# Kernel tuning notes

Hardware: AMD Instinct MI355X
Metric: run time of the kernel (lower is better)

## Reference

```python
import jax, jax.numpy as jnp
import numpy as np

B, C, L, H, W = 4, 128, 8, 64, 64

def setup_inputs() -> dict:
    key = jax.random.key(0)
    ks = jax.random.split(key, 9)
    s = 0.05
    return {
        'feats': jax.random.normal(ks[0], (B, C, L, H, W), jnp.float32),
        'proj_w': jax.random.normal(ks[1], (C, C, L), jnp.float32) * s,  # Conv3d kernel (band,1,1) collapsing l
        'proj_b': jax.random.normal(ks[2], (C,), jnp.float32) * s,
        'w1': jax.random.normal(ks[3], (C, C), jnp.float32) * s,
        'b1': jax.random.normal(ks[4], (C,), jnp.float32) * s,
        'w2': jax.random.normal(ks[5], (C, C), jnp.float32) * s,
        'b2': jax.random.normal(ks[6], (C,), jnp.float32) * s,
        'w3': jax.random.normal(ks[7], (C, C), jnp.float32) * s,
        'b3': jax.random.normal(ks[8], (C,), jnp.float32) * s,
        'alpha': jnp.zeros((1,), jnp.float32),
    }

def reference(feats, proj_w, proj_b, w1, b1, w2, b2, w3, b3, alpha):
    b, c, l, h, w = feats.shape
    hw = h * w
    # CVT3D_2D_SA: 3D->2D projection, conv3d kernel (l,1,1) then squeeze
    f2d = jnp.einsum('bclhw,ocl->bohw', feats, proj_w) + proj_b[None, :, None, None]
    # 1x1 conv projections -> (b, c, hw)
    x = f2d.reshape(b, c, hw)
    q = jnp.einsum('bcn,oc->bon', x, w1) + b1[None, :, None]
    k = jnp.einsum('bcn,oc->bon', x, w2) + b2[None, :, None]
    v = jnp.einsum('bcn,oc->bon', x, w3) + b3[None, :, None]
    # scores[b,n,m] = sum_c q[b,c,n] * k[b,c,m]; softmax over m (dim=-1)
    scores = jnp.einsum('bcn,bcm->bnm', q, k)
    attn = jax.nn.softmax(scores, axis=-1)
    # feat_e[b,c,n] = sum_m v[b,c,m] * attn[b,n,m]
    feat_e = jnp.einsum('bcm,bnm->bcn', v, attn).reshape(b, c, h, w)
    # original computes out = alpha*feat_e + f2d but returns feat_e
    return feat_e
```

## Files before the change

kernel.cpp:

```cpp
#include <hip/hip_runtime.h>
#include <stdint.h>

typedef _Float16 h8 __attribute__((ext_vector_type(8)));
typedef _Float16 h4 __attribute__((ext_vector_type(4)));
typedef float f32x4 __attribute__((ext_vector_type(4)));
typedef uint32_t u32x4 __attribute__((ext_vector_type(4)));

#if __has_builtin(__builtin_amdgcn_exp2f)
#define EXP2(x) __builtin_amdgcn_exp2f(x)
#else
#define EXP2(x) exp2f(x)
#endif

#define WS_PWH  0u
#define WS_WH   262144u
#define WS_BC   600064u
#define WS_F2D  1048576u
#define WS_OP   5242880u
#define WS_QKVT 38797312u
#define WS_VT   47185920u
#define WS_MLM  0u
#define WS_MLL  524288u

__device__ __forceinline__ void gll16(const void* g, void* l) {
  __builtin_amdgcn_global_load_lds((const __attribute__((address_space(1))) unsigned int*)g,
                                   (__attribute__((address_space(3))) unsigned int*)l, 16, 0, 0);
}

__global__ void k_cvt(const float* __restrict__ pw, const float* __restrict__ pb,
                      const float* __restrict__ w1, const float* __restrict__ b1,
                      const float* __restrict__ w2, const float* __restrict__ b2,
                      const float* __restrict__ w3, const float* __restrict__ b3,
                      _Float16* __restrict__ PWh, _Float16* __restrict__ Wh,
                      float* __restrict__ bc)
{
  const float LOG2E = 1.4426950408889634f;
  int idx = blockIdx.x * 256 + threadIdx.x;
  if (idx < 131072) {
    PWh[idx] = (_Float16)pw[idx];
  } else {
    int j = idx - 131072;
    if (j < 49152) {
      int g = j >> 14, rem = j & 16383;
      const float* wg = (g == 0) ? w1 : (g == 1 ? w2 : w3);
      float v = wg[rem];
      if (g == 0) v *= LOG2E;
      Wh[j] = (_Float16)v;
    }
  }
  if (idx < 384) {
    int g = idx >> 7, o = idx & 127;
    const float* wg = (g == 0) ? w1 : (g == 1 ? w2 : w3);
    const float* bg = (g == 0) ? b1 : (g == 1 ? b2 : b3);
    float s = bg[o];
    for (int c = 0; c < 128; ++c) s += wg[o * 128 + c] * pb[c];
    if (g == 0) s *= LOG2E;
    bc[idx] = s;
  }
}

#define FG1_LDS 51200
__global__ __launch_bounds__(256) void k_fg1(const float* __restrict__ feats,
                                             const _Float16* __restrict__ PWh,
                                             _Float16* __restrict__ f2d)
{
  extern __shared__ char smem[];
  const int t = threadIdx.x, lane = t & 63, w = t >> 6;
  const int lo = lane & 15, hi = lane >> 4;
  const int n0 = blockIdx.x * 32, b = blockIdx.y;
  const int wr = w >> 1, wc = w & 1;
  const char* pwc = (const char*)PWh;

  float4 areg[2];
  auto loadA = [&](int s) {
    #pragma unroll
    for (int p = 0; p < 2; ++p) {
      int i = t + p * 256, row = i >> 3, slot = i & 7;
      areg[p] = *(const float4*)(feats + ((size_t)(b * 1024 + s * 64 + row)) * 4096 + n0 + slot * 4);
    }
  };
  auto writeA = [&](int buf) {
    char* base = smem + buf * 9216;
    #pragma unroll
    for (int p = 0; p < 2; ++p) {
      int i = t + p * 256, row = i >> 3, slot = i & 7;
      *(float4*)(base + row * 144 + slot * 16) = areg[p];
    }
  };
  auto gllB = [&](int s, int buf) {
    char* base = smem + 18432 + buf * 16384;
    #pragma unroll
    for (int q = 0; q < 4; ++q) {
      int o = (w * 4 + q) * 8 + (lane >> 3);
      int slot = lane & 7;
      gll16(pwc + (size_t)o * 2048 + s * 128 + ((slot * 16) ^ ((o & 7) << 4)),
            base + (w * 4 + q) * 1024);
    }
  };

  const f32x4 zero4 = {0.f, 0.f, 0.f, 0.f};
  f32x4 acc[4];
  #pragma unroll
  for (int j2 = 0; j2 < 4; ++j2) acc[j2] = zero4;

  loadA(0); writeA(0); gllB(0, 0);
  for (int s = 0; s < 16; ++s) {
    __syncthreads();
    if (s < 15) { loadA(s + 1); gllB(s + 1, (s + 1) & 1); }
    const char* fb = smem + (s & 1) * 9216;
    const char* pb_ = smem + 18432 + (s & 1) * 16384;
    #pragma unroll
    for (int kk = 0; kk < 2; ++kk) {
      const int nl = wr * 16 + lo;
      float f0 = *(const float*)(fb + (kk * 32 + hi * 8 + 0) * 144 + nl * 4);
      float f1 = *(const float*)(fb + (kk * 32 + hi * 8 + 1) * 144 + nl * 4);
      float f2 = *(const float*)(fb + (kk * 32 + hi * 8 + 2) * 144 + nl * 4);
      float f3 = *(const float*)(fb + (kk * 32 + hi * 8 + 3) * 144 + nl * 4);
      float f4 = *(const float*)(fb + (kk * 32 + hi * 8 + 4) * 144 + nl * 4);
      float f5 = *(const float*)(fb + (kk * 32 + hi * 8 + 5) * 144 + nl * 4);
      float f6 = *(const float*)(fb + (kk * 32 + hi * 8 + 6) * 144 + nl * 4);
      float f7 = *(const float*)(fb + (kk * 32 + hi * 8 + 7) * 144 + nl * 4);
      u32x4 ua = { __builtin_bit_cast(uint32_t, __builtin_amdgcn_cvt_pkrtz(f0, f1)),
                   __builtin_bit_cast(uint32_t, __builtin_amdgcn_cvt_pkrtz(f2, f3)),
                   __builtin_bit_cast(uint32_t, __builtin_amdgcn_cvt_pkrtz(f4, f5)),
                   __builtin_bit_cast(uint32_t, __builtin_amdgcn_cvt_pkrtz(f6, f7)) };
      h8 af = __builtin_bit_cast(h8, ua);
      h8 bf[4];
      #pragma unroll
      for (int j2 = 0; j2 < 4; ++j2) {
        int o = wc * 64 + j2 * 16 + lo;
        bf[j2] = *(const h8*)(pb_ + o * 128 + ((kk * 64 + hi * 16) ^ ((o & 7) << 4)));
      }
      #pragma unroll
      for (int j2 = 0; j2 < 4; ++j2)
        acc[j2] = __builtin_amdgcn_mfma_f32_16x16x32_f16(af, bf[j2], acc[j2], 0, 0, 0);
    }
    if (s < 15) writeA((s + 1) & 1);
  }

  #pragma unroll
  for (int j2 = 0; j2 < 4; ++j2) {
    int o = wc * 64 + j2 * 16 + lo;
    #pragma unroll
    for (int r = 0; r < 4; ++r) {
      int n = n0 + wr * 16 + hi * 4 + r;
      f2d[((size_t)(b * 4096 + n)) * 128 + o] = (_Float16)acc[j2][r];
    }
  }
}

__global__ void k_gemm2(const _Float16* __restrict__ f2d, const _Float16* __restrict__ Wh,
                        const float* __restrict__ bc, _Float16* __restrict__ qkvt,
                        _Float16* __restrict__ vt)
{
  extern __shared__ char smem[];
  const int t = threadIdx.x, lane = t & 63, w = t >> 6;
  const int lo = lane & 15, hi = lane >> 4;
  const int bx = blockIdx.x, n0 = blockIdx.y * 128, b = blockIdx.z;
  const int wr = w >> 1, wc = w & 1;
  const int nb = wr * 64, ob = wc * 64;
  const char* f2c = (const char*)f2d;

  #pragma unroll
  for (int q = 0; q < 8; ++q) {
    int c = w * 8 + q;
    int row = c * 4 + (lane >> 4);
    int col = ((lane & 15) * 16) ^ ((row & 7) << 4);
    gll16(f2c + ((size_t)(b * 4096 + n0 + row)) * 256 + col, smem + c * 1024);
    gll16((const char*)Wh + (size_t)(bx * 128 + row) * 256 + col, smem + 32768 + c * 1024);
  }
  __syncthreads();

  const f32x4 zero4 = {0.f, 0.f, 0.f, 0.f};
  f32x4 acc[4][4];
  #pragma unroll
  for (int i2 = 0; i2 < 4; ++i2)
    #pragma unroll
    for (int j2 = 0; j2 < 4; ++j2) acc[i2][j2] = zero4;

  #pragma unroll
  for (int kk = 0; kk < 4; ++kk) {
    const int cb = kk * 64 + hi * 16;
    h8 af[4], bf[4];
    #pragma unroll
    for (int i2 = 0; i2 < 4; ++i2) {
      int row = nb + i2 * 16 + lo;
      af[i2] = *(const h8*)(smem + row * 256 + (cb ^ ((row & 7) << 4)));
    }
    #pragma unroll
    for (int j2 = 0; j2 < 4; ++j2) {
      int row = ob + j2 * 16 + lo;
      bf[j2] = *(const h8*)(smem + 32768 + row * 256 + (cb ^ ((row & 7) << 4)));
    }
    #pragma unroll
    for (int i2 = 0; i2 < 4; ++i2)
      #pragma unroll
      for (int j2 = 0; j2 < 4; ++j2)
        acc[i2][j2] = __builtin_amdgcn_mfma_f32_16x16x32_f16(af[i2], bf[j2], acc[i2][j2], 0, 0, 0);
  }

  if (bx < 2) {
    #pragma unroll
    for (int j2 = 0; j2 < 4; ++j2) {
      int o = bx * 128 + ob + j2 * 16 + lo;
      float bias = bc[o];
      #pragma unroll
      for (int i2 = 0; i2 < 4; ++i2)
        #pragma unroll
        for (int r = 0; r < 4; ++r) {
          int n = n0 + nb + i2 * 16 + hi * 4 + r;
          qkvt[((size_t)(b * 4096 + n)) * 256 + o] = (_Float16)(acc[i2][j2][r] + bias);
        }
    }
  } else {
    __syncthreads();
    #pragma unroll
    for (int j2 = 0; j2 < 4; ++j2) {
      int o = ob + j2 * 16 + lo;
      float bias = bc[256 + o];
      #pragma unroll
      for (int i2 = 0; i2 < 4; ++i2) {
        int nl = nb + i2 * 16 + hi * 4;
        h4 v4;
        #pragma unroll
        for (int r = 0; r < 4; ++r) v4[r] = (_Float16)(acc[i2][j2][r] + bias);
        *(h4*)(smem + o * 272 + nl * 2) = v4;
      }
    }
    __syncthreads();
    #pragma unroll
    for (int p2 = 0; p2 < 8; ++p2) {
      int i = t + p2 * 256, d = i >> 4, ch = i & 15;
      uint4 v = *(const uint4*)(smem + d * 272 + ch * 16);
      *(uint4*)((char*)vt + ((size_t)(b * 128 + d)) * 8192 + (n0 + ch * 8) * 2) = v;
    }
  }
}

#define ATT_LDS 65536
__global__ __launch_bounds__(512, 4) void k_attn_part(const _Float16* __restrict__ qkvt,
                                                      const _Float16* __restrict__ vt,
                                                      _Float16* __restrict__ opart,
                                                      float* __restrict__ mlm,
                                                      float* __restrict__ mll)
{
  extern __shared__ char smem[];
  const int t = threadIdx.x, lane = t & 63, w = t >> 6;
  const int lo = lane & 15, hi = lane >> 4;
  const int id = blockIdx.x;
  const int vid = (id & 7) * 128 + (id >> 3);
  const int qt = vid & 31, bp = vid >> 5;
  const int b = bp >> 3, p = bp & 7;
  const int n0 = qt * 128;
  const char* qbase = (const char*)qkvt + (size_t)b * 4096 * 512;
  const char* vbase = (const char*)vt + (size_t)b * 128 * 8192;

  h8 bq[4];
  {
    const char* qr = qbase + (size_t)(n0 + w * 16 + lo) * 512;
    #pragma unroll
    for (int dk = 0; dk < 4; ++dk) bq[dk] = *(const h8*)(qr + dk * 64 + hi * 16);
  }

  int koff[2], voff[2], dst_[2];
  #pragma unroll
  for (int q = 0; q < 2; ++q) {
    int c = w * 2 + q;
    int krow = c * 4 + (lane >> 4);
    koff[q] = krow * 512 + 256 + (((lane & 15) * 16) ^ ((krow & 7) << 4));
    int d = c * 8 + (lane >> 3);
    voff[q] = d * 8192 + (((lane & 7) * 16) ^ ((d & 7) << 4));
    dst_[q] = c * 1024;
  }

  auto stage = [&](int m0, int buf) {
    char* kb = smem + buf * 32768;
    char* vb = kb + 16384;
    #pragma unroll
    for (int q = 0; q < 2; ++q) {
      gll16(qbase + (size_t)m0 * 512 + koff[q], kb + dst_[q]);
      gll16(vbase + (size_t)m0 * 2 + voff[q], vb + dst_[q]);
    }
  };

  const f32x4 zero4 = {0.f, 0.f, 0.f, 0.f};
  float m_run = -1e30f, l_run = 0.f;
  f32x4 oacc[8];
  #pragma unroll
  for (int dt = 0; dt < 8; ++dt) oacc[dt] = zero4;

  const int slA = (hi & 1) * 32 + lo, slB = slA + 16;
  const bool up = (hi & 2) != 0;

  stage(p * 512, 0);
  __syncthreads();

  for (int it = 0; it < 8; ++it) {
    const int buf = it & 1;
    if (it < 7) stage(p * 512 + (it + 1) * 64, buf ^ 1);

    const char* kb = smem + buf * 32768;
    const char* vb = kb + 16384;

    f32x4 s[4];
    #pragma unroll
    for (int mt = 0; mt < 4; ++mt) s[mt] = zero4;
    __builtin_amdgcn_s_setprio(1);
    #pragma unroll
    for (int mt = 0; mt < 4; ++mt) {
      #pragma unroll
      for (int dk = 0; dk < 4; ++dk) {
        int row = mt * 16 + lo;
        h8 ak = *(const h8*)(kb + row * 256 + ((dk * 64 + hi * 16) ^ ((row & 7) << 4)));
        s[mt] = __builtin_amdgcn_mfma_f32_16x16x32_f16(ak, bq[dk], s[mt], 0, 0, 0);
      }
    }
    __builtin_amdgcn_s_setprio(0);

    float mxl = fmaxf(fmaxf(fmaxf(s[0][0], s[0][1]), fmaxf(s[0][2], s[0][3])),
                      fmaxf(fmaxf(s[1][0], s[1][1]), fmaxf(s[1][2], s[1][3])));
    mxl = fmaxf(mxl, fmaxf(fmaxf(fmaxf(s[2][0], s[2][1]), fmaxf(s[2][2], s[2][3])),
                           fmaxf(fmaxf(s[3][0], s[3][1]), fmaxf(s[3][2], s[3][3]))));
    if (__any(mxl > m_run + 8.f)) {
      float mq = fmaxf(mxl, __shfl_xor(mxl, 16));
      mq = fmaxf(mq, __shfl_xor(mq, 32));
      float mnew = fmaxf(m_run, mq);
      float scn = EXP2(m_run - mnew);
      m_run = mnew;
      l_run *= scn;
      #pragma unroll
      for (int dt = 0; dt < 8; ++dt) oacc[dt] *= scn;
    }

    uint32_t pk[4][2];
    float rs = 0.f;
    #pragma unroll
    for (int mt = 0; mt < 4; ++mt) {
      float p0 = EXP2(s[mt][0] - m_run), p1 = EXP2(s[mt][1] - m_run);
      float p2 = EXP2(s[mt][2] - m_run), p3 = EXP2(s[mt][3] - m_run);
      rs += (p0 + p1) + (p2 + p3);
      pk[mt][0] = __builtin_bit_cast(uint32_t, __builtin_amdgcn_cvt_pkrtz(p0, p1));
      pk[mt][1] = __builtin_bit_cast(uint32_t, __builtin_amdgcn_cvt_pkrtz(p2, p3));
    }
    l_run += rs;

    #pragma unroll
    for (int kk2 = 0; kk2 < 2; ++kk2) {
      uint32_t w0a = __shfl(pk[kk2 * 2][0], slA), w0b = __shfl(pk[kk2 * 2 + 1][0], slA);
      uint32_t w1a = __shfl(pk[kk2 * 2][1], slA), w1b = __shfl(pk[kk2 * 2 + 1][1], slA);
      uint32_t w2a = __shfl(pk[kk2 * 2][0], slB), w2b = __shfl(pk[kk2 * 2 + 1][0], slB);
      uint32_t w3a = __shfl(pk[kk2 * 2][1], slB), w3b = __shfl(pk[kk2 * 2 + 1][1], slB);
      u32x4 bw = { up ? w0b : w0a, up ? w1b : w1a, up ? w2b : w2a, up ? w3b : w3a };
      h8 bpf = __builtin_bit_cast(h8, bw);
      __builtin_amdgcn_s_setprio(1);
      #pragma unroll
      for (int dt = 0; dt < 8; ++dt) {
        int d = dt * 16 + lo;
        h8 av = *(const h8*)(vb + d * 128 + (((kk2 * 4 + hi) * 16) ^ ((d & 7) << 4)));
        oacc[dt] = __builtin_amdgcn_mfma_f32_16x16x32_f16(av, bpf, oacc[dt], 0, 0, 0);
      }
      __builtin_amdgcn_s_setprio(0);
    }

    if (it < 7) __syncthreads();
  }

  l_run += __shfl_xor(l_run, 16);
  l_run += __shfl_xor(l_run, 32);
  float invl = 1.0f / l_run;
  _Float16* oph = opart + ((size_t)(p * 4 + b) * 128) * 4096;
  const int ncol = n0 + w * 16 + lo;
  #pragma unroll
  for (int dt = 0; dt < 8; ++dt)
    #pragma unroll
    for (int r = 0; r < 4; ++r) {
      int d = dt * 16 + hi * 4 + r;
      oph[(size_t)d * 4096 + ncol] = (_Float16)(oacc[dt][r] * invl);
    }
  if (hi == 0) {
    size_t mlbase = (size_t)(p * 4 + b) * 4096 + ncol;
    mlm[mlbase] = m_run;
    mll[mlbase] = l_run;
  }
}

__global__ void k_reduce(const _Float16* __restrict__ opart, const float* __restrict__ mlm,
                         const float* __restrict__ mll, float* __restrict__ out)
{
  int idx = blockIdx.x * 256 + threadIdx.x;
  int n4 = idx & 1023, d = (idx >> 10) & 127, b = idx >> 17;
  int n0 = n4 * 4;
  f32x4 m[8], lv[8];
  #pragma unroll
  for (int p = 0; p < 8; ++p) {
    size_t mb = (size_t)(p * 4 + b) * 4096 + n0;
    m[p]  = *(const f32x4*)(mlm + mb);
    lv[p] = *(const f32x4*)(mll + mb);
  }
  f32x4 M = m[0];
  #pragma unroll
  for (int p = 1; p < 8; ++p)
    #pragma unroll
    for (int j = 0; j < 4; ++j) M[j] = fmaxf(M[j], m[p][j]);
  f32x4 denom = {0.f, 0.f, 0.f, 0.f}, num = {0.f, 0.f, 0.f, 0.f};
  #pragma unroll
  for (int p = 0; p < 8; ++p) {
    h4 o = *(const h4*)(opart + ((size_t)((p * 4 + b) * 128 + d)) * 4096 + n0);
    #pragma unroll
    for (int j = 0; j < 4; ++j) {
      float wgt = lv[p][j] * EXP2(m[p][j] - M[j]);
      denom[j] += wgt;
      num[j]   += (float)o[j] * wgt;
    }
  }
  f32x4 r;
  #pragma unroll
  for (int j = 0; j < 4; ++j) r[j] = num[j] / denom[j];
  *(f32x4*)(out + ((size_t)(b * 128 + d)) * 4096 + n0) = r;
}

extern "C" void kernel_launch(void* const* d_in, const int* in_sizes, int n_in,
                              void* d_out, int out_size, void* d_ws, size_t ws_size,
                              hipStream_t stream)
{
  const float* feats = (const float*)d_in[0];
  const float* pw = (const float*)d_in[1];
  const float* pb = (const float*)d_in[2];
  const float* w1 = (const float*)d_in[3];
  const float* b1 = (const float*)d_in[4];
  const float* w2 = (const float*)d_in[5];
  const float* b2 = (const float*)d_in[6];
  const float* w3 = (const float*)d_in[7];
  const float* b3 = (const float*)d_in[8];
  char* ws = (char*)d_ws;
  _Float16* PWh = (_Float16*)(ws + WS_PWH);
  _Float16* Wh = (_Float16*)(ws + WS_WH);
  float* bc = (float*)(ws + WS_BC);
  _Float16* f2d = (_Float16*)(ws + WS_F2D);
  _Float16* qkvt = (_Float16*)(ws + WS_QKVT);
  _Float16* vt = (_Float16*)(ws + WS_VT);
  _Float16* opart = (_Float16*)(ws + WS_OP);
  float* mlm = (float*)(ws + WS_MLM);
  float* mll = (float*)(ws + WS_MLL);
  float* out = (float*)d_out;

  hipLaunchKernelGGL(k_cvt, dim3(704), dim3(256), 0, stream,
                     pw, pb, w1, b1, w2, b2, w3, b3, PWh, Wh, bc);
  hipLaunchKernelGGL(k_fg1, dim3(128, 4), dim3(256), FG1_LDS, stream, feats, PWh, f2d);
  hipLaunchKernelGGL(k_gemm2, dim3(3, 32, 4), dim3(256), 65536, stream, f2d, Wh, bc, qkvt, vt);
  hipLaunchKernelGGL(k_attn_part, dim3(1024), dim3(512), ATT_LDS, stream, qkvt, vt, opart, mlm, mll);
  hipLaunchKernelGGL(k_reduce, dim3(2048), dim3(256), 0, stream, opart, mlm, mll, out);
}
```

Baseline: 108.1 us.

## Software-pipeline attention loop with 32-key tiles and triple-buffered K

Restructures the attention partial kernel to process 32-key tiles instead of 64, triple-buffering K and double-buffering V in a smaller LDS footprint. The QK^T MFMAs for the next tile are issued before the softmax and PV of the current tile, so matrix work overlaps the exponentials and shuffles. The LDS swizzle and staging layout are rewritten so each thread issues one 16-byte load per operand. This doubles the number of iterations and barriers, adds register pressure from the extra score accumulators, and the smaller LDS use may allow more blocks per CU.

```diff
diff --git a/kernel.cpp b/kernel.cpp
--- a/kernel.cpp
+++ b/kernel.cpp
@@ -237,7 +237,7 @@
   }
 }
 
-#define ATT_LDS 65536
+#define ATT_LDS 40960
 __global__ __launch_bounds__(512, 4) void k_attn_part(const _Float16* __restrict__ qkvt,
                                                       const _Float16* __restrict__ vt,
                                                       _Float16* __restrict__ opart,
@@ -262,25 +262,18 @@
     for (int dk = 0; dk < 4; ++dk) bq[dk] = *(const h8*)(qr + dk * 64 + hi * 16);
   }
 
-  int koff[2], voff[2], dst_[2];
-  #pragma unroll
-  for (int q = 0; q < 2; ++q) {
-    int c = w * 2 + q;
-    int krow = c * 4 + (lane >> 4);
-    koff[q] = krow * 512 + 256 + (((lane & 15) * 16) ^ ((krow & 7) << 4));
-    int d = c * 8 + (lane >> 3);
-    voff[q] = d * 8192 + (((lane & 7) * 16) ^ ((d & 7) << 4));
-    dst_[q] = c * 1024;
-  }
-
-  auto stage = [&](int m0, int buf) {
-    char* kb = smem + buf * 32768;
-    char* vb = kb + 16384;
-    #pragma unroll
-    for (int q = 0; q < 2; ++q) {
-      gll16(qbase + (size_t)m0 * 512 + koff[q], kb + dst_[q]);
-      gll16(vbase + (size_t)m0 * 2 + voff[q], vb + dst_[q]);
-    }
+  const int kr_ = t >> 4;
+  const int koff = kr_ * 512 + 256 + (((t & 15) ^ (kr_ & 15)) * 16);
+  const int vlo = (t >> 2) & 15;
+  const int vd_ = (t >> 6) * 16 + vlo;
+  const int voff = vd_ * 8192 + (((t & 3) ^ (vlo & 3)) * 16);
+  const int dst16 = t * 16;
+
+  auto stageK = [&](int m0, char* kb) {
+    gll16(qbase + (size_t)m0 * 512 + koff, kb + dst16);
+  };
+  auto stageV = [&](int m0, char* vb) {
+    gll16(vbase + (size_t)m0 * 2 + voff, vb + dst16);
   };
 
   const f32x4 zero4 = {0.f, 0.f, 0.f, 0.f};
@@ -288,39 +281,45 @@
   f32x4 oacc[8];
   #pragma unroll
   for (int dt = 0; dt < 8; ++dt) oacc[dt] = zero4;
+  f32x4 s_cur[2], s_next[2];
 
   const int slA = (hi & 1) * 32 + lo, slB = slA + 16;
   const bool up = (hi & 2) != 0;
 
-  stage(p * 512, 0);
-  __syncthreads();
-
-  for (int it = 0; it < 8; ++it) {
-    const int buf = it & 1;
-    if (it < 7) stage(p * 512 + (it + 1) * 64, buf ^ 1);
-
-    const char* kb = smem + buf * 32768;
-    const char* vb = kb + 16384;
-
-    f32x4 s[4];
-    #pragma unroll
-    for (int mt = 0; mt < 4; ++mt) s[mt] = zero4;
+  char* kb0 = smem;
+  char* kb1 = smem + 8192;
+  char* kb2 = smem + 16384;
+  char* vb0 = smem + 24576;
+  char* vb1 = smem + 32768;
+
+  const int base = p * 512;
+
+  auto qk = [&](const char* kb, f32x4* sv) {
+    sv[0] = zero4; sv[1] = zero4;
     __builtin_amdgcn_s_setprio(1);
     #pragma unroll
-    for (int mt = 0; mt < 4; ++mt) {
+    for (int mt = 0; mt < 2; ++mt) {
       #pragma unroll
       for (int dk = 0; dk < 4; ++dk) {
         int row = mt * 16 + lo;
-        h8 ak = *(const h8*)(kb + row * 256 + ((dk * 64 + hi * 16) ^ ((row & 7) << 4)));
-        s[mt] = __builtin_amdgcn_mfma_f32_16x16x32_f16(ak, bq[dk], s[mt], 0, 0, 0);
+        h8 ak = *(const h8*)(kb + row * 256 + (((dk * 4 + hi) ^ lo) * 16));
+        sv[mt] = __builtin_amdgcn_mfma_f32_16x16x32_f16(ak, bq[dk], sv[mt], 0, 0, 0);
       }
     }
     __builtin_amdgcn_s_setprio(0);
-
-    float mxl = fmaxf(fmaxf(fmaxf(s[0][0], s[0][1]), fmaxf(s[0][2], s[0][3])),
-                      fmaxf(fmaxf(s[1][0], s[1][1]), fmaxf(s[1][2], s[1][3])));
-    mxl = fmaxf(mxl, fmaxf(fmaxf(fmaxf(s[2][0], s[2][1]), fmaxf(s[2][2], s[2][3])),
-                           fmaxf(fmaxf(s[3][0], s[3][1]), fmaxf(s[3][2], s[3][3]))));
+  };
+
+  stageK(base, kb0); stageV(base, vb0); stageK(base + 32, kb1);
+  __syncthreads();
+  qk(kb0, s_cur);
+
+  for (int it = 0; it < 16; ++it) {
+    if (it < 14) stageK(base + (it + 2) * 32, kb2);
+    if (it < 15) stageV(base + (it + 1) * 32, vb1);
+    if (it < 15) qk(kb1, s_next);
+
+    float mxl = fmaxf(fmaxf(fmaxf(s_cur[0][0], s_cur[0][1]), fmaxf(s_cur[0][2], s_cur[0][3])),
+                      fmaxf(fmaxf(s_cur[1][0], s_cur[1][1]), fmaxf(s_cur[1][2], s_cur[1][3])));
     if (__any(mxl > m_run + 8.f)) {
       float mq = fmaxf(mxl, __shfl_xor(mxl, 16));
       mq = fmaxf(mq, __shfl_xor(mq, 32));
@@ -331,38 +330,39 @@
       #pragma unroll
       for (int dt = 0; dt < 8; ++dt) oacc[dt] *= scn;
     }
-
-    uint32_t pk[4][2];
+    uint32_t pk[2][2];
     float rs = 0.f;
     #pragma unroll
-    for (int mt = 0; mt < 4; ++mt) {
-      float p0 = EXP2(s[mt][0] - m_run), p1 = EXP2(s[mt][1] - m_run);
-      float p2 = EXP2(s[mt][2] - m_run), p3 = EXP2(s[mt][3] - m_run);
+    for (int mt = 0; mt < 2; ++mt) {
+      float p0 = EXP2(s_cur[mt][0] - m_run), p1 = EXP2(s_cur[mt][1] - m_run);
+      float p2 = EXP2(s_cur[mt][2] - m_run), p3 = EXP2(s_cur[mt][3] - m_run);
       rs += (p0 + p1) + (p2 + p3);
       pk[mt][0] = __builtin_bit_cast(uint32_t, __builtin_amdgcn_cvt_pkrtz(p0, p1));
       pk[mt][1] = __builtin_bit_cast(uint32_t, __builtin_amdgcn_cvt_pkrtz(p2, p3));
     }
     l_run += rs;
 
-    #pragma unroll
-    for (int kk2 = 0; kk2 < 2; ++kk2) {
-      uint32_t w0a = __shfl(pk[kk2 * 2][0], slA), w0b = __shfl(pk[kk2 * 2 + 1][0], slA);
-      uint32_t w1a = __shfl(pk[kk2 * 2][1], slA), w1b = __shfl(pk[kk2 * 2 + 1][1], slA);
-      uint32_t w2a = __shfl(pk[kk2 * 2][0], slB), w2b = __shfl(pk[kk2 * 2 + 1][0], slB);
-      uint32_t w3a = __shfl(pk[kk2 * 2][1], slB), w3b = __shfl(pk[kk2 * 2 + 1][1], slB);
-      u32x4 bw = { up ? w0b : w0a, up ? w1b : w1a, up ? w2b : w2a, up ? w3b : w3a };
-      h8 bpf = __builtin_bit_cast(h8, bw);
-      __builtin_amdgcn_s_setprio(1);
-      #pragma unroll
-      for (int dt = 0; dt < 8; ++dt) {
-        int d = dt * 16 + lo;
-        h8 av = *(const h8*)(vb + d * 128 + (((kk2 * 4 + hi) * 16) ^ ((d & 7) << 4)));
-        oacc[dt] = __builtin_amdgcn_mfma_f32_16x16x32_f16(av, bpf, oacc[dt], 0, 0, 0);
-      }
-      __builtin_amdgcn_s_setprio(0);
-    }
-
-    if (it < 7) __syncthreads();
+    uint32_t w0a = __shfl(pk[0][0], slA), w0b = __shfl(pk[1][0], slA);
+    uint32_t w1a = __shfl(pk[0][1], slA), w1b = __shfl(pk[1][1], slA);
+    uint32_t w2a = __shfl(pk[0][0], slB), w2b = __shfl(pk[1][0], slB);
+    uint32_t w3a = __shfl(pk[0][1], slB), w3b = __shfl(pk[1][1], slB);
+    u32x4 bw = { up ? w0b : w0a, up ? w1b : w1a, up ? w2b : w2a, up ? w3b : w3a };
+    h8 bpf = __builtin_bit_cast(h8, bw);
+
+    __builtin_amdgcn_s_setprio(1);
+    #pragma unroll
+    for (int dt = 0; dt < 8; ++dt) {
+      h8 av = *(const h8*)(vb0 + lo * 64 + ((hi ^ (lo & 3)) * 16) + dt * 1024);
+      oacc[dt] = __builtin_amdgcn_mfma_f32_16x16x32_f16(av, bpf, oacc[dt], 0, 0, 0);
+    }
+    __builtin_amdgcn_s_setprio(0);
+
+    if (it < 15) {
+      __syncthreads();
+      s_cur[0] = s_next[0]; s_cur[1] = s_next[1];
+      char* tmp = kb0; kb0 = kb1; kb1 = kb2; kb2 = tmp;
+      char* tv = vb0; vb0 = vb1; vb1 = tv;
+    }
   }
 
   l_run += __shfl_xor(l_run, 16);
```

Measured after the change: 109.0 us. Within noise of the previous version (+0.9%).

## Switch attention kernel to 32x32x16 MFMA with 4-wave blocks and 32-key tiles

Applied to the files above, without the earlier changes.

Rewrites the split-KV attention kernel to use 32x32x16 f16 MFMA instead of 16x16x32. Each of 4 waves now owns 32 query rows, and K/V tiles shrink to 32 keys staged over 16 iterations with new LDS swizzles. The P fragment is rebuilt with a single xor-32 shuffle instead of many indexed shuffles. This is meant to cut LDS reads and shuffle work per flop, but it doubles the number of barrier and softmax-rescale steps and raises per-thread accumulator register pressure.

```diff
diff --git a/kernel.cpp b/kernel.cpp
--- a/kernel.cpp
+++ b/kernel.cpp
@@ -4,6 +4,7 @@
 typedef _Float16 h8 __attribute__((ext_vector_type(8)));
 typedef _Float16 h4 __attribute__((ext_vector_type(4)));
 typedef float f32x4 __attribute__((ext_vector_type(4)));
+typedef float f32x16 __attribute__((ext_vector_type(16)));
 typedef uint32_t u32x4 __attribute__((ext_vector_type(4)));
 
 #if __has_builtin(__builtin_amdgcn_exp2f)
@@ -237,8 +238,8 @@
   }
 }
 
-#define ATT_LDS 65536
-__global__ __launch_bounds__(512, 4) void k_attn_part(const _Float16* __restrict__ qkvt,
+#define ATT_LDS 32768
+__global__ __launch_bounds__(256, 2) void k_attn_part(const _Float16* __restrict__ qkvt,
                                                       const _Float16* __restrict__ vt,
                                                       _Float16* __restrict__ opart,
                                                       float* __restrict__ mlm,
@@ -246,7 +247,7 @@
 {
   extern __shared__ char smem[];
   const int t = threadIdx.x, lane = t & 63, w = t >> 6;
-  const int lo = lane & 15, hi = lane >> 4;
+  const int q31 = lane & 31, h2 = lane >> 5;
   const int id = blockIdx.x;
   const int vid = (id & 7) * 128 + (id >> 3);
   const int qt = vid & 31, bp = vid >> 5;
@@ -255,129 +256,125 @@
   const char* qbase = (const char*)qkvt + (size_t)b * 4096 * 512;
   const char* vbase = (const char*)vt + (size_t)b * 128 * 8192;
 
-  h8 bq[4];
+  h8 bq[8];
   {
-    const char* qr = qbase + (size_t)(n0 + w * 16 + lo) * 512;
-    #pragma unroll
-    for (int dk = 0; dk < 4; ++dk) bq[dk] = *(const h8*)(qr + dk * 64 + hi * 16);
+    const char* qr = qbase + (size_t)(n0 + w * 32 + q31) * 512;
+    #pragma unroll
+    for (int dk = 0; dk < 8; ++dk) bq[dk] = *(const h8*)(qr + dk * 32 + h2 * 16);
   }
 
   int koff[2], voff[2], dst_[2];
   #pragma unroll
-  for (int q = 0; q < 2; ++q) {
-    int c = w * 2 + q;
-    int krow = c * 4 + (lane >> 4);
-    koff[q] = krow * 512 + 256 + (((lane & 15) * 16) ^ ((krow & 7) << 4));
-    int d = c * 8 + (lane >> 3);
-    voff[q] = d * 8192 + (((lane & 7) * 16) ^ ((d & 7) << 4));
-    dst_[q] = c * 1024;
+  for (int i = 0; i < 2; ++i) {
+    int idx = t + i * 256;
+    int krow = idx >> 4, ks = idx & 15;
+    koff[i] = krow * 512 + 256 + ((ks ^ (krow & 7)) * 16);
+    int vd = idx >> 2, vs = idx & 3;
+    voff[i] = vd * 8192 + ((vs ^ ((vd >> 1) & 3)) * 16);
+    dst_[i] = idx * 16;
   }
 
   auto stage = [&](int m0, int buf) {
-    char* kb = smem + buf * 32768;
-    char* vb = kb + 16384;
-    #pragma unroll
-    for (int q = 0; q < 2; ++q) {
-      gll16(qbase + (size_t)m0 * 512 + koff[q], kb + dst_[q]);
-      gll16(vbase + (size_t)m0 * 2 + voff[q], vb + dst_[q]);
+    char* kb = smem + buf * 16384;
+    char* vb = kb + 8192;
+    #pragma unroll
+    for (int i = 0; i < 2; ++i) {
+      gll16(qbase + (size_t)m0 * 512 + koff[i], kb + dst_[i]);
+      gll16(vbase + (size_t)m0 * 2 + voff[i], vb + dst_[i]);
     }
   };
 
-  const f32x4 zero4 = {0.f, 0.f, 0.f, 0.f};
   float m_run = -1e30f, l_run = 0.f;
-  f32x4 oacc[8];
-  #pragma unroll
-  for (int dt = 0; dt < 8; ++dt) oacc[dt] = zero4;
-
-  const int slA = (hi & 1) * 32 + lo, slB = slA + 16;
-  const bool up = (hi & 2) != 0;
-
-  stage(p * 512, 0);
+  f32x16 oacc[4];
+  #pragma unroll
+  for (int dt = 0; dt < 4; ++dt)
+    #pragma unroll
+    for (int r = 0; r < 16; ++r) oacc[dt][r] = 0.f;
+
+  const int base = p * 512;
+  stage(base, 0);
   __syncthreads();
 
-  for (int it = 0; it < 8; ++it) {
+  for (int it = 0; it < 16; ++it) {
     const int buf = it & 1;
-    if (it < 7) stage(p * 512 + (it + 1) * 64, buf ^ 1);
-
-    const char* kb = smem + buf * 32768;
-    const char* vb = kb + 16384;
-
-    f32x4 s[4];
-    #pragma unroll
-    for (int mt = 0; mt < 4; ++mt) s[mt] = zero4;
+    if (it < 15) stage(base + (it + 1) * 32, buf ^ 1);
+
+    const char* kb = smem + buf * 16384;
+    const char* vb = kb + 8192;
+
+    f32x16 s;
+    #pragma unroll
+    for (int r = 0; r < 16; ++r) s[r] = 0.f;
     __builtin_amdgcn_s_setprio(1);
     #pragma unroll
-    for (int mt = 0; mt < 4; ++mt) {
-      #pragma unroll
-      for (int dk = 0; dk < 4; ++dk) {
-        int row = mt * 16 + lo;
-        h8 ak = *(const h8*)(kb + row * 256 + ((dk * 64 + hi * 16) ^ ((row & 7) << 4)));
-        s[mt] = __builtin_amdgcn_mfma_f32_16x16x32_f16(ak, bq[dk], s[mt], 0, 0, 0);
-      }
+    for (int dk = 0; dk < 8; ++dk) {
+      h8 ak = *(const h8*)(kb + q31 * 256 + (((dk * 2 + h2) ^ (q31 & 7)) * 16));
+      s = __builtin_amdgcn_mfma_f32_32x32x16_f16(ak, bq[dk], s, 0, 0, 0);
     }
     __builtin_amdgcn_s_setprio(0);
 
-    float mxl = fmaxf(fmaxf(fmaxf(s[0][0], s[0][1]), fmaxf(s[0][2], s[0][3])),
-                      fmaxf(fmaxf(s[1][0], s[1][1]), fmaxf(s[1][2], s[1][3])));
-    mxl = fmaxf(mxl, fmaxf(fmaxf(fmaxf(s[2][0], s[2][1]), fmaxf(s[2][2], s[2][3])),
-                           fmaxf(fmaxf(s[3][0], s[3][1]), fmaxf(s[3][2], s[3][3]))));
+    float mxl = s[0];
+    #pragma unroll
+    for (int r = 1; r < 16; ++r) mxl = fmaxf(mxl, s[r]);
     if (__any(mxl > m_run + 8.f)) {
-      float mq = fmaxf(mxl, __shfl_xor(mxl, 16));
-      mq = fmaxf(mq, __shfl_xor(mq, 32));
+      float mq = fmaxf(mxl, __shfl_xor(mxl, 32));
       float mnew = fmaxf(m_run, mq);
       float scn = EXP2(m_run - mnew);
       m_run = mnew;
       l_run *= scn;
       #pragma unroll
-      for (int dt = 0; dt < 8; ++dt) oacc[dt] *= scn;
-    }
-
-    uint32_t pk[4][2];
+      for (int dt = 0; dt < 4; ++dt)
+        #pragma unroll
+        for (int r = 0; r < 16; ++r) oacc[dt][r] *= scn;
+    }
+    float pv[16];
     float rs = 0.f;
     #pragma unroll
-    for (int mt = 0; mt < 4; ++mt) {
-      float p0 = EXP2(s[mt][0] - m_run), p1 = EXP2(s[mt][1] - m_run);
-      float p2 = EXP2(s[mt][2] - m_run), p3 = EXP2(s[mt][3] - m_run);
-      rs += (p0 + p1) + (p2 + p3);
-      pk[mt][0] = __builtin_bit_cast(uint32_t, __builtin_amdgcn_cvt_pkrtz(p0, p1));
-      pk[mt][1] = __builtin_bit_cast(uint32_t, __builtin_amdgcn_cvt_pkrtz(p2, p3));
-    }
+    for (int r = 0; r < 16; ++r) { pv[r] = EXP2(s[r] - m_run); rs += pv[r]; }
     l_run += rs;
-
-    #pragma unroll
-    for (int kk2 = 0; kk2 < 2; ++kk2) {
-      uint32_t w0a = __shfl(pk[kk2 * 2][0], slA), w0b = __shfl(pk[kk2 * 2 + 1][0], slA);
-      uint32_t w1a = __shfl(pk[kk2 * 2][1], slA), w1b = __shfl(pk[kk2 * 2 + 1][1], slA);
-      uint32_t w2a = __shfl(pk[kk2 * 2][0], slB), w2b = __shfl(pk[kk2 * 2 + 1][0], slB);
-      uint32_t w3a = __shfl(pk[kk2 * 2][1], slB), w3b = __shfl(pk[kk2 * 2 + 1][1], slB);
-      u32x4 bw = { up ? w0b : w0a, up ? w1b : w1a, up ? w2b : w2a, up ? w3b : w3a };
-      h8 bpf = __builtin_bit_cast(h8, bw);
-      __builtin_amdgcn_s_setprio(1);
-      #pragma unroll
-      for (int dt = 0; dt < 8; ++dt) {
-        int d = dt * 16 + lo;
-        h8 av = *(const h8*)(vb + d * 128 + (((kk2 * 4 + hi) * 16) ^ ((d & 7) << 4)));
-        oacc[dt] = __builtin_amdgcn_mfma_f32_16x16x32_f16(av, bpf, oacc[dt], 0, 0, 0);
+    uint32_t wd[8];
+    #pragma unroll
+    for (int j = 0; j < 8; ++j)
+      wd[j] = __builtin_bit_cast(uint32_t, __builtin_amdgcn_cvt_pkrtz(pv[2 * j], pv[2 * j + 1]));
+
+    uint32_t xw[8];
+    #pragma unroll
+    for (int j = 0; j < 8; ++j) xw[j] = __shfl_xor(wd[j], 32);
+    u32x4 b0 = { h2 ? xw[2] : wd[0], h2 ? xw[3] : wd[1],
+                 h2 ? wd[2] : xw[0], h2 ? wd[3] : xw[1] };
+    u32x4 b1 = { h2 ? xw[6] : wd[4], h2 ? xw[7] : wd[5],
+                 h2 ? wd[6] : xw[4], h2 ? wd[7] : xw[5] };
+    h8 bp0 = __builtin_bit_cast(h8, b0);
+    h8 bp1 = __builtin_bit_cast(h8, b1);
+
+    __builtin_amdgcn_s_setprio(1);
+    #pragma unroll
+    for (int ks = 0; ks < 2; ++ks) {
+      h8 bpf = ks ? bp1 : bp0;
+      #pragma unroll
+      for (int dt = 0; dt < 4; ++dt) {
+        int d = dt * 32 + q31;
+        h8 av = *(const h8*)(vb + d * 64 + (((ks * 2 + h2) ^ ((d >> 1) & 3)) * 16));
+        oacc[dt] = __builtin_amdgcn_mfma_f32_32x32x16_f16(av, bpf, oacc[dt], 0, 0, 0);
       }
-      __builtin_amdgcn_s_setprio(0);
-    }
-
-    if (it < 7) __syncthreads();
-  }
-
-  l_run += __shfl_xor(l_run, 16);
+    }
+    __builtin_amdgcn_s_setprio(0);
+
+    if (it < 15) __syncthreads();
+  }
+
   l_run += __shfl_xor(l_run, 32);
   float invl = 1.0f / l_run;
   _Float16* oph = opart + ((size_t)(p * 4 + b) * 128) * 4096;
-  const int ncol = n0 + w * 16 + lo;
-  #pragma unroll
-  for (int dt = 0; dt < 8; ++dt)
-    #pragma unroll
-    for (int r = 0; r < 4; ++r) {
-      int d = dt * 16 + hi * 4 + r;
+  const int ncol = n0 + w * 32 + q31;
+  #pragma unroll
+  for (int dt = 0; dt < 4; ++dt)
+    #pragma unroll
+    for (int r = 0; r < 16; ++r) {
+      int d = dt * 32 + (r & 3) + 8 * (r >> 2) + 4 * h2;
       oph[(size_t)d * 4096 + ncol] = (_Float16)(oacc[dt][r] * invl);
     }
-  if (hi == 0) {
+  if (h2 == 0) {
     size_t mlbase = (size_t)(p * 4 + b) * 4096 + ncol;
     mlm[mlbase] = m_run;
     mll[mlbase] = l_run;
@@ -448,6 +445,6 @@
                      pw, pb, w1, b1, w2, b2, w3, b3, PWh, Wh, bc);
   hipLaunchKernelGGL(k_fg1, dim3(128, 4), dim3(256), FG1_LDS, stream, feats, PWh, f2d);
   hipLaunchKernelGGL(k_gemm2, dim3(3, 32, 4), dim3(256), 65536, stream, f2d, Wh, bc, qkvt, vt);
-  hipLaunchKernelGGL(k_attn_part, dim3(1024), dim3(512), ATT_LDS, stream, qkvt, vt, opart, mlm, mll);
+  hipLaunchKernelGGL(k_attn_part, dim3(1024), dim3(256), ATT_LDS, stream, qkvt, vt, opart, mlm, mll);
   hipLaunchKernelGGL(k_reduce, dim3(2048), dim3(256), 0, stream, opart, mlm, mll, out);
 }
```

Measured after the change: 106.8 us. No clear change (-1.1%).
